# Optimization experiments

Hardware: AMD Instinct MI355X
Metric: run time of the kernel (lower is better)

Reference implementation:

```python
import jax, jax.numpy as jnp
import numpy as np

# NSA hyperparams (match init_kwargs)
D_BLK = 64    # d: block stride
L_CMP = 64    # compression block length (== d -> non-overlapping blocks)
L_SLC = 64    # selection block length (== l_cmp == d -> P_slc = P_cmp)
BQ = 64       # block_size_q
TOPK = 16     # slc_top_k
WL, WR = 512, 0  # sliding window (left, right)


def _nsa_forward(q, k, v, w_k, b_k, w_v, b_v, w_gate, b_gate, seqlen):
    S, qh, dim = q.shape
    kv = k.shape[1]
    H = qh // kv
    b = S // seqlen          # number of equal-length packed sequences
    s = seqlen
    scale = dim ** -0.5
    f32 = jnp.float32

    # [b, s, kv, H, e]: q head g*H+h belongs to kv head g (repeat_interleave layout)
    q5 = q.reshape(b, s, kv, H, dim)
    k3 = k.reshape(b, s, kv, dim)
    v3 = v.reshape(b, s, kv, dim)

    # ---- block compression (extract_blocks + cmp_linear over block length) ----
    n_blk = s // D_BLK
    kb = k.reshape(b, n_blk, D_BLK, kv, dim)
    vb = v.reshape(b, n_blk, D_BLK, kv, dim)
    K_cmp = jnp.einsum('bntke,t->bnke', kb, w_k) + b_k[0]
    V_cmp = jnp.einsum('bntke,t->bnke', vb, w_v) + b_v[0]

    # ---- compressed attention (per sequence, fp32 softmax) ----
    sc = jnp.einsum('bqkhe,bnke->bkhqn', q5, K_cmp).astype(f32) * scale
    P = jax.nn.softmax(sc, axis=-1)
    out_cmp = jnp.einsum('bkhqn,bnke->bqkhe', P.astype(q.dtype), V_cmp)

    # ---- selection scores: pool P over q-blocks and GQA groups, then top-k ----
    nqb = s // BQ
    pooled = P.reshape(b, kv, H, nqb, BQ, n_blk).sum(axis=(2, 4))  # [b,kv,nqb,n_blk]
    idx = jax.lax.top_k(pooled, TOPK)[1]                            # [b,kv,nqb,TOPK]

    # gather selected K/V blocks (shared by all queries in a q-block / GQA group)
    kb2 = jnp.transpose(kb, (0, 3, 1, 2, 4))  # [b,kv,n_blk,l,e]
    vb2 = jnp.transpose(vb, (0, 3, 1, 2, 4))
    gather = jax.vmap(jax.vmap(lambda blocks, i: blocks[i]))
    K_sel = gather(kb2, idx)  # [b,kv,nqb,TOPK,l,e]
    V_sel = gather(vb2, idx)

    # ---- selected-block attention ----
    qblk = q5.reshape(b, nqb, BQ, kv, H, dim)
    sc2 = jnp.einsum('bnckhe,bkntle->bkhnctl', qblk, K_sel).astype(f32) * scale
    sc2 = sc2.reshape(b, kv, H, nqb, BQ, TOPK * L_SLC)
    P2 = jax.nn.softmax(sc2, axis=-1).astype(q.dtype)
    out_slc = jnp.einsum('bkhncm,bknme->bnckhe', P2,
                         V_sel.reshape(b, kv, nqb, TOPK * L_SLC, dim))
    out_slc = out_slc.reshape(b, s, kv, H, dim)

    # ---- sliding-window attention (window_size=(WL, WR), non-causal flag) ----
    sw = jnp.einsum('bikhe,bjke->bkhij', q5, k3).astype(f32) * scale
    i = jnp.arange(s)[:, None]
    j = jnp.arange(s)[None, :]
    valid = (j >= i - WL) & (j <= i + WR)
    sw = jnp.where(valid, sw, -jnp.inf)
    Pw = jax.nn.softmax(sw, axis=-1).astype(q.dtype)
    out_win = jnp.einsum('bkhij,bjke->bikhe', Pw, v3)

    # ---- gated fusion of the three branches ----
    gate = jax.nn.sigmoid(jnp.einsum('bqkhe,ec->bqkhc', q5, w_gate) + b_gate)
    out = (gate[..., 0:1] * out_cmp
           + gate[..., 1:2] * out_slc
           + gate[..., 2:3] * out_win)
    return out.reshape(S, qh, dim)


def setup_inputs() -> dict:
    key = jax.random.key(0)
    ks = jax.random.split(key, 9)
    S, qh, kvh, dim = 4096, 8, 2, 128
    inp = {
        'q': jax.random.normal(ks[0], (S, qh, dim), jnp.float32),
        'k': jax.random.normal(ks[1], (S, kvh, dim), jnp.float32),
        'v': jax.random.normal(ks[2], (S, kvh, dim), jnp.float32),
        'w_k': jax.random.normal(ks[3], (L_CMP,), jnp.float32) * (L_CMP ** -0.5),
        'b_k': jax.random.normal(ks[4], (1,), jnp.float32) * 0.02,
        'w_v': jax.random.normal(ks[5], (L_CMP,), jnp.float32) * (L_CMP ** -0.5),
        'b_v': jax.random.normal(ks[6], (1,), jnp.float32) * 0.02,
        'w_gate': jax.random.normal(ks[7], (dim, 3), jnp.float32) * (dim ** -0.5),
        'b_gate': jax.random.normal(ks[8], (3,), jnp.float32) * 0.02,
        'seqlen': 2048,
    }
    return inp


def reference(q, k, v, w_k, b_k, w_v, b_v, w_gate, b_gate, seqlen):
    return _nsa_forward(q, k, v, w_k, b_k, w_v, b_v, w_gate, b_gate, seqlen)
```

## Files before the change

kernel.cpp:

```cpp
#include <hip/hip_runtime.h>
#include <hip/hip_bf16.h>


#define SEQ   2048
#define NB    2
#define KV    2
#define NH    4
#define QH    8
#define DIM   128
#define NBLK  32
#define NQB   32
#define NTOP  16
#define SCALE 0.08838834764831845f
#define QS    36
#define RS    144
#define QP    136
#define VP    72

typedef unsigned short ushort_t;
using bf16x8 = __attribute__((ext_vector_type(8))) short;
using f32x4  = __attribute__((ext_vector_type(4))) float;

__device__ __forceinline__ unsigned pkbf(float a, float b){
  union { __hip_bfloat162 h; unsigned u; } cv;
  cv.h = __float22bfloat162_rn(make_float2(a, b));
  return cv.u;
}
__device__ __forceinline__ ushort_t f2b(float f){
  union { float f; unsigned i; } x; x.f = f;
  unsigned r = x.i + 0x7fffu + ((x.i >> 16) & 1u);
  return (ushort_t)(r >> 16);
}

__global__ __launch_bounds__(256) void prep_k(
    const float* __restrict__ k, const float* __restrict__ v,
    ushort_t* __restrict__ Kb, ushort_t* __restrict__ VT)
{
  int blk = blockIdx.x;
  int db = blk & 1, rb = (blk >> 1) & 31, bbg = blk >> 6;
  int bb = bbg >> 1, g = bbg & 1;
  int tid = threadIdx.x;
  __shared__ ushort_t T[64*VP];

  for (int jj = 0; jj < 4; ++jj){
    int i = tid + jj*256;
    int r = i >> 4, ds = i & 15;
    size_t src = ((size_t)(bb*SEQ + rb*64 + r)*KV + g)*DIM + db*64 + ds*4;
    float4 kx = *(const float4*)(k + src);
    float4 vx = *(const float4*)(v + src);
    uint2 kk; kk.x = pkbf(kx.x,kx.y); kk.y = pkbf(kx.z,kx.w);
    *(uint2*)&Kb[((size_t)bbg*SEQ + rb*64 + r)*DIM + db*64 + ds*4] = kk;
    unsigned v01 = pkbf(vx.x,vx.y), v23 = pkbf(vx.z,vx.w);
    T[(ds*4+0)*VP + r] = (ushort_t)(v01 & 0xffffu);
    T[(ds*4+1)*VP + r] = (ushort_t)(v01 >> 16);
    T[(ds*4+2)*VP + r] = (ushort_t)(v23 & 0xffffu);
    T[(ds*4+3)*VP + r] = (ushort_t)(v23 >> 16);
  }
  __syncthreads();
  for (int jj = 0; jj < 4; ++jj){
    int i = tid + jj*256;
    int d = i >> 4, seg = i & 15;
    uint2 u = *(uint2*)&T[d*VP + seg*4];
    *(uint2*)&VT[((size_t)bbg*DIM + db*64 + d)*SEQ + rb*64 + seg*4] = u;
  }
}

__global__ __launch_bounds__(256) void compress_k(
    const float* __restrict__ k, const float* __restrict__ v,
    const float* __restrict__ w_k, const float* __restrict__ b_k,
    const float* __restrict__ w_v, const float* __restrict__ b_v,
    float* __restrict__ Kc, float* __restrict__ Vc)
{
  int blk = blockIdx.x;
  int dh = blk & 1;
  int n  = (blk >> 1) & 31;
  int g  = (blk >> 6) & 1;
  int bb = blk >> 7;
  int tid = threadIdx.x;

  __shared__ float wks[64], wvs[64];
  __shared__ float accK[16][64], accV[16][64];
  if (tid < 64){ wks[tid] = w_k[tid]; wvs[tid] = w_v[tid]; }
  __syncthreads();

  int r4 = tid >> 4, dq = tid & 15;
  float4 sk = {0,0,0,0}, sv = {0,0,0,0};
  for (int rr = 0; rr < 4; ++rr){
    int row = r4*4 + rr;
    size_t off = ((size_t)(bb*SEQ + n*64 + row)*KV + g)*DIM + dh*64 + dq*4;
    float4 kx = *(const float4*)(k + off);
    float4 vx = *(const float4*)(v + off);
    float a = wks[row], b = wvs[row];
    sk.x += a*kx.x; sk.y += a*kx.y; sk.z += a*kx.z; sk.w += a*kx.w;
    sv.x += b*vx.x; sv.y += b*vx.y; sv.z += b*vx.z; sv.w += b*vx.w;
  }
  *(float4*)&accK[r4][dq*4] = sk;
  *(float4*)&accV[r4][dq*4] = sv;
  __syncthreads();
  size_t obase = ((size_t)((bb*KV+g)*NBLK + n))*DIM + dh*64;
  if (tid < 64){
    float s = 0.f;
#pragma unroll
    for (int i = 0; i < 16; ++i) s += accK[i][tid];
    Kc[obase + tid] = s + b_k[0];
  } else if (tid < 128){
    int d = tid - 64;
    float s = 0.f;
#pragma unroll
    for (int i = 0; i < 16; ++i) s += accV[i][d];
    Vc[obase + d] = s + b_v[0];
  }
}

__global__ __launch_bounds__(256) void cmp_attn_k(
    const float* __restrict__ q, const float* __restrict__ Kc,
    const float* __restrict__ Vc,
    const float* __restrict__ w_gate, const float* __restrict__ b_gate,
    float* __restrict__ pooled_part, float* __restrict__ out)
{
  int blk = blockIdx.x;
  int h  = blk & 3;
  int qb = (blk >> 2) & (NQB-1);
  int g  = (blk >> 7) & 1;
  int bb = blk >> 8;
  int tid = threadIdx.x;
  int qi = tid >> 2, c = tid & 3;

  __shared__ float Ks[32*RS];
  __shared__ float Vs[32*RS];
  __shared__ float wsum[4][NBLK];

  const float4* Ksrc = (const float4*)(Kc + (size_t)(bb*KV + g) * NBLK * DIM);
  const float4* Vsrc = (const float4*)(Vc + (size_t)(bb*KV + g) * NBLK * DIM);
  for (int i = tid; i < 1024; i += 256){
    int row = i >> 5, seg = i & 31;
    int dst = row*RS + (seg>>3)*QS + (seg&7)*4;
    ((float4*)(Ks+dst))[0] = Ksrc[i];
    ((float4*)(Vs+dst))[0] = Vsrc[i];
  }
  __syncthreads();

  int row = bb*SEQ + qb*64 + qi;
  float qv[32];
  {
    const float4* q4 = (const float4*)(q + ((size_t)row*QH + g*NH + h)*DIM + c*32);
#pragma unroll
    for (int j = 0; j < 8; ++j){
      float4 u = q4[j];
      qv[4*j+0]=u.x; qv[4*j+1]=u.y; qv[4*j+2]=u.z; qv[4*j+3]=u.w;
    }
  }

  float gp = 0.f;
#pragma unroll
  for (int d = 0; d < 32; ++d) gp += qv[d]*w_gate[(c*32+d)*3 + 0];
  gp += __shfl_xor(gp, 1); gp += __shfl_xor(gp, 2);
  float g0 = 1.f/(1.f + expf(-(gp + b_gate[0])));

  float sc[NBLK];
#pragma unroll
  for (int n = 0; n < NBLK; ++n){
    float p = 0.f;
    const float4* kr = (const float4*)(Ks + n*RS + c*QS);
#pragma unroll
    for (int j = 0; j < 8; ++j){
      float4 u = kr[j];
      p += qv[4*j+0]*u.x + qv[4*j+1]*u.y + qv[4*j+2]*u.z + qv[4*j+3]*u.w;
    }
    p += __shfl_xor(p, 1); p += __shfl_xor(p, 2);
    sc[n] = p * SCALE;
  }
  float m = sc[0];
#pragma unroll
  for (int n = 1; n < NBLK; ++n) m = fmaxf(m, sc[n]);
  float l = 0.f;
#pragma unroll
  for (int n = 0; n < NBLK; ++n){ sc[n] = expf(sc[n]-m); l += sc[n]; }
  float inv = 1.f/l;
#pragma unroll
  for (int n = 0; n < NBLK; ++n) sc[n] *= inv;

#pragma unroll
  for (int n = 0; n < NBLK; ++n){
    float t2 = sc[n];
    t2 += __shfl_xor(t2, 4); t2 += __shfl_xor(t2, 8);
    t2 += __shfl_xor(t2, 16); t2 += __shfl_xor(t2, 32);
    if ((tid & 63) == 0) wsum[tid>>6][n] = t2;
  }
  __syncthreads();
  if (tid < NBLK)
    pooled_part[(size_t)blk*NBLK + tid] =
        (wsum[0][tid]+wsum[1][tid]) + (wsum[2][tid]+wsum[3][tid]);

  float o[32];
#pragma unroll
  for (int d = 0; d < 32; ++d) o[d] = 0.f;
#pragma unroll
  for (int n = 0; n < NBLK; ++n){
    float pb = sc[n];
    const float4* vr = (const float4*)(Vs + n*RS + c*QS);
#pragma unroll
    for (int j = 0; j < 8; ++j){
      float4 u = vr[j];
      o[4*j+0] += pb*u.x; o[4*j+1] += pb*u.y;
      o[4*j+2] += pb*u.z; o[4*j+3] += pb*u.w;
    }
  }
  float* op = out + ((size_t)row*QH + g*NH + h)*DIM + c*32;
#pragma unroll
  for (int d = 0; d < 32; ++d) op[d] = g0*o[d];
}

__global__ __launch_bounds__(256, 3) void attn_k(
    const float* __restrict__ q, const ushort_t* __restrict__ Kb,
    const ushort_t* __restrict__ VT, const float* __restrict__ pp,
    const float* __restrict__ w_gate, const float* __restrict__ b_gate,
    float* __restrict__ slcbuf, float* __restrict__ out)
{
  int idx = blockIdx.x;
  int x = idx & 7, low = idx & 1, u = idx >> 3;
  int bbg = x >> 1;
  int j = u*2 + low;
  int role = j >> 7;
  int qb = (j >> 2) & 31;
  int h  = j & 3;
  int bb = bbg >> 1, g = bbg & 1;

  int tid = threadIdx.x;
  int lane = tid & 63, w = tid >> 6, quad = lane >> 4, l15 = lane & 15;

  __shared__ short Ks[64*QP];
  __shared__ short VTs[128*VP];
  __shared__ short Ps[64*VP];
  __shared__ float gbuf[64];
  __shared__ int   idxs[NTOP];

  if (role == 0 && tid < 64){
    int n = lane;
    float val = -INFINITY;
    if (n < NBLK){
      const float* p0 = pp + ((size_t)((bb*KV+g)*NQB + qb)*NH)*NBLK + n;
      val = (p0[0] + p0[NBLK]) + (p0[2*NBLK] + p0[3*NBLK]);
    }
    for (int t = 0; t < NTOP; ++t){
      float bv = val; int bi = n;
      for (int mm = 1; mm < 32; mm <<= 1){
        float ov = __shfl_xor(bv, mm);
        int   oi = __shfl_xor(bi, mm);
        if (ov > bv || (ov == bv && oi < bi)){ bv = ov; bi = oi; }
      }
      if (lane == 0) idxs[t] = bi;
      if (n == bi) val = -INFINITY;
    }
  }

  const float* qrow = q + ((size_t)(bb*SEQ + qb*64 + w*16 + l15)*QH + g*NH + h)*DIM;
  int gcol = 1 + role;
  bf16x8 qfrag[4];
  float gp = 0.f;
#pragma unroll
  for (int kc = 0; kc < 4; ++kc){
    int d0 = kc*32 + quad*8;
    float4 u0 = *(const float4*)(qrow + d0);
    float4 u1 = *(const float4*)(qrow + d0 + 4);
    float qf[8] = {u0.x,u0.y,u0.z,u0.w,u1.x,u1.y,u1.z,u1.w};
#pragma unroll
    for (int jj = 0; jj < 8; ++jj) gp += qf[jj]*w_gate[(d0+jj)*3 + gcol];
    union { unsigned uu[4]; bf16x8 v8; } tq;
    tq.uu[0] = pkbf(u0.x,u0.y); tq.uu[1] = pkbf(u0.z,u0.w);
    tq.uu[2] = pkbf(u1.x,u1.y); tq.uu[3] = pkbf(u1.z,u1.w);
    qfrag[kc] = tq.v8;
  }
  gp += __shfl_xor(gp,16); gp += __shfl_xor(gp,32);
  if (quad == 0) gbuf[w*16+l15] = 1.f/(1.f + __expf(-(gp + b_gate[gcol])));
  __syncthreads();
  float gl[4];
#pragma unroll
  for (int r = 0; r < 4; ++r) gl[r] = gbuf[w*16+quad*4+r];

  const ushort_t* kbase = Kb + (size_t)bbg*SEQ*DIM;
  const ushort_t* vtbase = VT + (size_t)bbg*DIM*SEQ;

  int kb0 = (qb >= 8) ? (qb - 8) : 0;
  int nph = (role == 0) ? NTOP : (qb - kb0 + 1);

  float m1[4], l1[4];
  f32x4 oacc[8];
  const f32x4 zero4 = {0.f,0.f,0.f,0.f};
#pragma unroll
  for (int r = 0; r < 4; ++r){ m1[r] = -INFINITY; l1[r] = 0.f; }
#pragma unroll
  for (int dt = 0; dt < 8; ++dt) oacc[dt] = zero4;

  for (int t = 0; t < nph; ++t){
    int kb = (role == 0) ? idxs[t] : (kb0 + t);
    __syncthreads();
    {
      const ushort_t* ksrc = kbase + (size_t)kb*64*DIM;
#pragma unroll
      for (int jj = 0; jj < 4; ++jj){
        int i = tid + jj*256;
        int row = i >> 4, seg = i & 15;
        uint4 uu = *(const uint4*)(ksrc + row*DIM + seg*8);
        *(uint4*)&Ks[row*QP + seg*8] = uu;
      }
      const ushort_t* vsrc = vtbase + kb*64;
#pragma unroll
      for (int jj = 0; jj < 4; ++jj){
        int i = tid + jj*256;
        int dr = i >> 3, seg = i & 7;
        uint4 uu = *(const uint4*)(vsrc + (size_t)dr*SEQ + seg*8);
        *(uint4*)&VTs[dr*VP + seg*8] = uu;
      }
    }
    __syncthreads();

    f32x4 sacc[4];
#pragma unroll
    for (int nt = 0; nt < 4; ++nt) sacc[nt] = zero4;
#pragma unroll
    for (int kc = 0; kc < 4; ++kc){
      bf16x8 a = qfrag[kc];
#pragma unroll
      for (int nt = 0; nt < 4; ++nt){
        bf16x8 b = *(bf16x8*)&Ks[(nt*16 + l15)*QP + kc*32 + quad*8];
        sacc[nt] = __builtin_amdgcn_mfma_f32_16x16x32_bf16(a, b, sacc[nt], 0, 0, 0);
      }
    }

    bool mlow  = (role == 1) && (kb == qb - 8);
    bool mhigh = (role == 1) && (kb == qb);
    float alpha[4];
#pragma unroll
    for (int r = 0; r < 4; ++r){
      int qi_local = w*16 + quad*4 + r;
      float mx = -INFINITY;
#pragma unroll
      for (int nt = 0; nt < 4; ++nt){
        int key = nt*16 + l15;
        float sv = sacc[nt][r]*SCALE;
        bool valid = (!mlow || key >= qi_local) && (!mhigh || key <= qi_local);
        sv = valid ? sv : -INFINITY;
        sacc[nt][r] = sv;
        mx = fmaxf(mx, sv);
      }
      mx = fmaxf(mx, __shfl_xor(mx,1)); mx = fmaxf(mx, __shfl_xor(mx,2));
      mx = fmaxf(mx, __shfl_xor(mx,4)); mx = fmaxf(mx, __shfl_xor(mx,8));
      float mn = fmaxf(m1[r], mx);
      alpha[r] = __expf(m1[r] - mn);
      float s0 = 0.f;
#pragma unroll
      for (int nt = 0; nt < 4; ++nt){
        float pe = __expf(sacc[nt][r] - mn);
        sacc[nt][r] = pe;
        s0 += pe;
      }
      s0 += __shfl_xor(s0,1); s0 += __shfl_xor(s0,2);
      s0 += __shfl_xor(s0,4); s0 += __shfl_xor(s0,8);
      l1[r] = l1[r]*alpha[r] + s0;
      m1[r] = mn;
    }
#pragma unroll
    for (int nt = 0; nt < 4; ++nt)
#pragma unroll
      for (int r = 0; r < 4; ++r)
        Ps[(w*16 + quad*4 + r)*VP + nt*16 + l15] = (short)f2b(sacc[nt][r]);
#pragma unroll
    for (int dt = 0; dt < 8; ++dt)
#pragma unroll
      for (int r = 0; r < 4; ++r) oacc[dt][r] *= alpha[r];
#pragma unroll
    for (int kc2 = 0; kc2 < 2; ++kc2){
      bf16x8 pa = *(bf16x8*)&Ps[(w*16 + l15)*VP + kc2*32 + quad*8];
#pragma unroll
      for (int dt = 0; dt < 8; ++dt){
        bf16x8 vb8 = *(bf16x8*)&VTs[(dt*16 + l15)*VP + kc2*32 + quad*8];
        oacc[dt] = __builtin_amdgcn_mfma_f32_16x16x32_bf16(pa, vb8, oacc[dt], 0, 0, 0);
      }
    }
  }

#pragma unroll
  for (int r = 0; r < 4; ++r){
    float s2 = gl[r] / l1[r];
    size_t ob = ((size_t)(bb*SEQ + qb*64 + w*16 + quad*4 + r)*QH + g*NH + h)*DIM + l15;
    if (role == 0){
      float* op = slcbuf + ob;
#pragma unroll
      for (int dt = 0; dt < 8; ++dt) op[dt*16] = s2 * oacc[dt][r];
    } else {
      float* op = out + ob;
#pragma unroll
      for (int dt = 0; dt < 8; ++dt) op[dt*16] += s2 * oacc[dt][r];
    }
  }
}

__global__ __launch_bounds__(256) void merge_k(const float* __restrict__ slcbuf,
                                               float* __restrict__ out){
  int i = blockIdx.x * 256 + threadIdx.x;
  float4 a = ((const float4*)slcbuf)[i];
  float4 b = ((float4*)out)[i];
  b.x += a.x; b.y += a.y; b.z += a.z; b.w += a.w;
  ((float4*)out)[i] = b;
}

extern "C" void kernel_launch(void* const* d_in, const int* in_sizes, int n_in,
                              void* d_out, int out_size, void* d_ws, size_t ws_size,
                              hipStream_t stream) {
  const float* q      = (const float*)d_in[0];
  const float* k      = (const float*)d_in[1];
  const float* v      = (const float*)d_in[2];
  const float* w_k    = (const float*)d_in[3];
  const float* b_k    = (const float*)d_in[4];
  const float* w_v    = (const float*)d_in[5];
  const float* b_v    = (const float*)d_in[6];
  const float* w_gate = (const float*)d_in[7];
  const float* b_gate = (const float*)d_in[8];
  float* out = (float*)d_out;

  float* ws     = (float*)d_ws;
  float* Kc     = ws;
  float* Vc     = ws + 16384;
  float* pp     = ws + 32768;
  float* slcbuf = ws + 49152;
  ushort_t* Kb  = (ushort_t*)(ws + 4243456);
  ushort_t* VT  = Kb + 1048576;

  prep_k    <<<256, 256, 0, stream>>>(k, v, Kb, VT);
  compress_k<<<256, 256, 0, stream>>>(k, v, w_k, b_k, w_v, b_v, Kc, Vc);
  cmp_attn_k<<<NB*KV*NQB*NH, 256, 0, stream>>>(q, Kc, Vc, w_gate, b_gate, pp, out);
  attn_k    <<<1024, 256, 0, stream>>>(q, Kb, VT, pp, w_gate, b_gate, slcbuf, out);
  merge_k   <<<4096, 256, 0, stream>>>(slcbuf, out);
}
```

Baseline: 198.6 us.

## Pre-swizzle K/V into MFMA fragment layout and load operands directly from global

```diff
diff --git a/kernel.cpp b/kernel.cpp
--- a/kernel.cpp
+++ b/kernel.cpp
@@ -14,8 +14,8 @@
 #define SCALE 0.08838834764831845f
 #define QS    36
 #define RS    144
-#define QP    136
 #define VP    72
+#define TP    72
 
 typedef unsigned short ushort_t;
 using bf16x8 = __attribute__((ext_vector_type(8))) short;
@@ -34,34 +34,55 @@
 
 __global__ __launch_bounds__(256) void prep_k(
     const float* __restrict__ k, const float* __restrict__ v,
-    ushort_t* __restrict__ Kb, ushort_t* __restrict__ VT)
+    ushort_t* __restrict__ Kfrag, ushort_t* __restrict__ Vfrag)
 {
   int blk = blockIdx.x;
-  int db = blk & 1, rb = (blk >> 1) & 31, bbg = blk >> 6;
+  int n = blk & 31, bbg = blk >> 5;
   int bb = bbg >> 1, g = bbg & 1;
   int tid = threadIdx.x;
-  __shared__ ushort_t T[64*VP];
-
+  __shared__ ushort_t TT[128*TP];
+
+  size_t kout = ((size_t)(bbg*NBLK + n)*16)*64*8;
+#pragma unroll
   for (int jj = 0; jj < 4; ++jj){
+    int o = tid + jj*256;
+    int f = o >> 6, l = o & 63;
+    int kc = f >> 2, nt = f & 3;
+    int key = nt*16 + (l & 15);
+    int d0  = kc*32 + (l >> 4)*8;
+    const float* src = k + ((size_t)(bb*SEQ + n*64 + key)*KV + g)*DIM + d0;
+    float4 u0 = *(const float4*)src;
+    float4 u1 = *(const float4*)(src + 4);
+    uint4 pk;
+    pk.x = pkbf(u0.x,u0.y); pk.y = pkbf(u0.z,u0.w);
+    pk.z = pkbf(u1.x,u1.y); pk.w = pkbf(u1.z,u1.w);
+    *(uint4*)&Kfrag[kout + (size_t)o*8] = pk;
+  }
+
+#pragma unroll
+  for (int jj = 0; jj < 8; ++jj){
     int i = tid + jj*256;
-    int r = i >> 4, ds = i & 15;
-    size_t src = ((size_t)(bb*SEQ + rb*64 + r)*KV + g)*DIM + db*64 + ds*4;
-    float4 kx = *(const float4*)(k + src);
+    int key = i >> 5, ds = i & 31;
+    size_t src = ((size_t)(bb*SEQ + n*64 + key)*KV + g)*DIM + ds*4;
     float4 vx = *(const float4*)(v + src);
-    uint2 kk; kk.x = pkbf(kx.x,kx.y); kk.y = pkbf(kx.z,kx.w);
-    *(uint2*)&Kb[((size_t)bbg*SEQ + rb*64 + r)*DIM + db*64 + ds*4] = kk;
     unsigned v01 = pkbf(vx.x,vx.y), v23 = pkbf(vx.z,vx.w);
-    T[(ds*4+0)*VP + r] = (ushort_t)(v01 & 0xffffu);
-    T[(ds*4+1)*VP + r] = (ushort_t)(v01 >> 16);
-    T[(ds*4+2)*VP + r] = (ushort_t)(v23 & 0xffffu);
-    T[(ds*4+3)*VP + r] = (ushort_t)(v23 >> 16);
-  }
-  __syncthreads();
+    TT[(ds*4+0)*TP + key] = (ushort_t)(v01 & 0xffffu);
+    TT[(ds*4+1)*TP + key] = (ushort_t)(v01 >> 16);
+    TT[(ds*4+2)*TP + key] = (ushort_t)(v23 & 0xffffu);
+    TT[(ds*4+3)*TP + key] = (ushort_t)(v23 >> 16);
+  }
+  __syncthreads();
+
+  size_t vout = ((size_t)(bbg*NBLK + n)*16)*64*8;
+#pragma unroll
   for (int jj = 0; jj < 4; ++jj){
-    int i = tid + jj*256;
-    int d = i >> 4, seg = i & 15;
-    uint2 u = *(uint2*)&T[d*VP + seg*4];
-    *(uint2*)&VT[((size_t)bbg*DIM + db*64 + d)*SEQ + rb*64 + seg*4] = u;
+    int o = tid + jj*256;
+    int f = o >> 6, l = o & 63;
+    int kc2 = f >> 3, dt = f & 7;
+    int d    = dt*16 + (l & 15);
+    int key0 = kc2*32 + (l >> 4)*8;
+    uint4 u = *(uint4*)&TT[d*TP + key0];
+    *(uint4*)&Vfrag[vout + (size_t)o*8] = u;
   }
 }
 
@@ -211,9 +232,9 @@
   for (int d = 0; d < 32; ++d) op[d] = g0*o[d];
 }
 
-__global__ __launch_bounds__(256, 3) void attn_k(
-    const float* __restrict__ q, const ushort_t* __restrict__ Kb,
-    const ushort_t* __restrict__ VT, const float* __restrict__ pp,
+__global__ __launch_bounds__(256, 2) void attn_k(
+    const float* __restrict__ q, const ushort_t* __restrict__ Kfrag,
+    const ushort_t* __restrict__ Vfrag, const float* __restrict__ pp,
     const float* __restrict__ w_gate, const float* __restrict__ b_gate,
     float* __restrict__ slcbuf, float* __restrict__ out)
 {
@@ -229,8 +250,6 @@
   int tid = threadIdx.x;
   int lane = tid & 63, w = tid >> 6, quad = lane >> 4, l15 = lane & 15;
 
-  __shared__ short Ks[64*QP];
-  __shared__ short VTs[128*VP];
   __shared__ short Ps[64*VP];
   __shared__ float gbuf[64];
   __shared__ int   idxs[NTOP];
@@ -278,8 +297,8 @@
 #pragma unroll
   for (int r = 0; r < 4; ++r) gl[r] = gbuf[w*16+quad*4+r];
 
-  const ushort_t* kbase = Kb + (size_t)bbg*SEQ*DIM;
-  const ushort_t* vtbase = VT + (size_t)bbg*DIM*SEQ;
+  const bf16x8* kfb = (const bf16x8*)Kfrag + (size_t)bbg*NBLK*16*64;
+  const bf16x8* vfb = (const bf16x8*)Vfrag + (size_t)bbg*NBLK*16*64;
 
   int kb0 = (qb >= 8) ? (qb - 8) : 0;
   int nph = (role == 0) ? NTOP : (qb - kb0 + 1);
@@ -294,26 +313,8 @@
 
   for (int t = 0; t < nph; ++t){
     int kb = (role == 0) ? idxs[t] : (kb0 + t);
-    __syncthreads();
-    {
-      const ushort_t* ksrc = kbase + (size_t)kb*64*DIM;
-#pragma unroll
-      for (int jj = 0; jj < 4; ++jj){
-        int i = tid + jj*256;
-        int row = i >> 4, seg = i & 15;
-        uint4 uu = *(const uint4*)(ksrc + row*DIM + seg*8);
-        *(uint4*)&Ks[row*QP + seg*8] = uu;
-      }
-      const ushort_t* vsrc = vtbase + kb*64;
-#pragma unroll
-      for (int jj = 0; jj < 4; ++jj){
-        int i = tid + jj*256;
-        int dr = i >> 3, seg = i & 7;
-        uint4 uu = *(const uint4*)(vsrc + (size_t)dr*SEQ + seg*8);
-        *(uint4*)&VTs[dr*VP + seg*8] = uu;
-      }
-    }
-    __syncthreads();
+    const bf16x8* kf = kfb + (size_t)kb*16*64;
+    const bf16x8* vf = vfb + (size_t)kb*16*64;
 
     f32x4 sacc[4];
 #pragma unroll
@@ -323,7 +324,7 @@
       bf16x8 a = qfrag[kc];
 #pragma unroll
       for (int nt = 0; nt < 4; ++nt){
-        bf16x8 b = *(bf16x8*)&Ks[(nt*16 + l15)*QP + kc*32 + quad*8];
+        bf16x8 b = kf[(kc*4+nt)*64 + lane];
         sacc[nt] = __builtin_amdgcn_mfma_f32_16x16x32_bf16(a, b, sacc[nt], 0, 0, 0);
       }
     }
@@ -374,7 +375,7 @@
       bf16x8 pa = *(bf16x8*)&Ps[(w*16 + l15)*VP + kc2*32 + quad*8];
 #pragma unroll
       for (int dt = 0; dt < 8; ++dt){
-        bf16x8 vb8 = *(bf16x8*)&VTs[(dt*16 + l15)*VP + kc2*32 + quad*8];
+        bf16x8 vb8 = vf[(kc2*8+dt)*64 + lane];
         oacc[dt] = __builtin_amdgcn_mfma_f32_16x16x32_bf16(pa, vb8, oacc[dt], 0, 0, 0);
       }
     }
@@ -419,17 +420,17 @@
   const float* b_gate = (const float*)d_in[8];
   float* out = (float*)d_out;
 
-  float* ws     = (float*)d_ws;
-  float* Kc     = ws;
-  float* Vc     = ws + 16384;
-  float* pp     = ws + 32768;
-  float* slcbuf = ws + 49152;
-  ushort_t* Kb  = (ushort_t*)(ws + 4243456);
-  ushort_t* VT  = Kb + 1048576;
-
-  prep_k    <<<256, 256, 0, stream>>>(k, v, Kb, VT);
+  float* ws       = (float*)d_ws;
+  float* Kc       = ws;
+  float* Vc       = ws + 16384;
+  float* pp       = ws + 32768;
+  float* slcbuf   = ws + 49152;
+  ushort_t* Kfrag = (ushort_t*)(ws + 4243456);
+  ushort_t* Vfrag = Kfrag + 1048576;
+
+  prep_k    <<<128, 256, 0, stream>>>(k, v, Kfrag, Vfrag);
   compress_k<<<256, 256, 0, stream>>>(k, v, w_k, b_k, w_v, b_v, Kc, Vc);
   cmp_attn_k<<<NB*KV*NQB*NH, 256, 0, stream>>>(q, Kc, Vc, w_gate, b_gate, pp, out);
-  attn_k    <<<1024, 256, 0, stream>>>(q, Kb, VT, pp, w_gate, b_gate, slcbuf, out);
+  attn_k    <<<1024, 256, 0, stream>>>(q, Kfrag, Vfrag, pp, w_gate, b_gate, slcbuf, out);
   merge_k   <<<4096, 256, 0, stream>>>(slcbuf, out);
 }
```

After: 210.2 us. 5.8% more time.
